# Optimization experiments

Hardware: AMD Instinct MI355X
Metric: run time of the kernel (lower is better)

## Reference

```python
import jax, jax.numpy as jnp
import numpy as np

LN_EPS = 1e-5
RMS_EPS = 1e-5

B, T, D = 4, 2048, 1024
H, DK, DV = 4, 256, 512            # head_k_dim = D/H, head_v_dim = expand_v * head_k_dim (expand_v=2)
KDIM, VDIM = H * DK, H * DV        # 1024, 2048
FFN = 4096                          # int(d_model * ffn_ratio)
CONV = 4


def _layernorm(x, w, b):
    mu = jnp.mean(x, -1, keepdims=True)
    var = jnp.mean(jnp.square(x - mu), -1, keepdims=True)
    return (x - mu) * jax.lax.rsqrt(var + LN_EPS) * w + b


def _short_conv_silu(x, w):
    # causal depthwise conv, kernel size K, then SiLU. x: [B,T,C], w: [C,K]
    K = w.shape[1]
    xp = jnp.pad(x, ((0, 0), (K - 1, 0), (0, 0)))
    y = sum(xp[:, i:i + x.shape[1], :] * w[:, i] for i in range(K))
    return jax.nn.silu(y)


def _l2norm(x):
    return x * jax.lax.rsqrt(jnp.sum(jnp.square(x), -1, keepdims=True) + 1e-6)


def _gated_delta_rule(q, k, v, g, beta):
    # q,k: [B,T,H,DK]; v: [B,T,H,DV]; g,beta: [B,T,H]
    # S_t = exp(g_t)*S_{t-1} + k_t (beta_t*(v_t - k_t^T exp(g_t) S_{t-1}))^T ; o_t = q_t^T S_t
    def step(S, inp):
        qt, kt, vt, gt, bt = inp
        S = S * jnp.exp(gt)[..., None, None]          # [B,H,DK,DV]
        mem = jnp.einsum('bhk,bhkv->bhv', kt, S)
        delta = (vt - mem) * bt[..., None]
        S = S + jnp.einsum('bhk,bhv->bhkv', kt, delta)
        o = jnp.einsum('bhk,bhkv->bhv', qt, S)
        return S, o
    S0 = jnp.zeros((q.shape[0], H, DK, DV), q.dtype)
    xs = (q.transpose(1, 0, 2, 3), k.transpose(1, 0, 2, 3), v.transpose(1, 0, 2, 3),
          g.transpose(1, 0, 2), beta.transpose(1, 0, 2))
    _, o = jax.lax.scan(step, S0, xs)
    return o.transpose(1, 0, 2, 3)  # [B,T,H,DV]


def setup_inputs() -> dict:
    key = jax.random.key(0)
    ks = jax.random.split(key, 24)
    n = lambda k, shp, s=0.02: jax.random.normal(k, shp, dtype=jnp.float32) * s
    return {
        'x': jax.random.normal(ks[0], (B, T, D), dtype=jnp.float32),
        'Wq': n(ks[1], (D, KDIM)), 'Wk': n(ks[2], (D, KDIM)), 'Wv': n(ks[3], (D, VDIM)),
        'Wa': n(ks[4], (D, H)), 'Wb': n(ks[5], (D, H)), 'Wg': n(ks[6], (D, VDIM)),
        'conv_q_w': n(ks[7], (KDIM, CONV), 0.2), 'conv_k_w': n(ks[8], (KDIM, CONV), 0.2),
        'conv_v_w': n(ks[9], (VDIM, CONV), 0.2),
        'A_log': jnp.log(jax.random.uniform(ks[10], (H,), minval=1.0, maxval=16.0, dtype=jnp.float32)),
        'dt_bias': jax.random.uniform(ks[11], (H,), minval=0.0, maxval=0.5, dtype=jnp.float32),
        'o_norm_w': jnp.ones((DV,), jnp.float32),
        'Wo': n(ks[12], (VDIM, D)),
        'ln1_w': jnp.ones((D,), jnp.float32), 'ln1_b': jnp.zeros((D,), jnp.float32),
        'ln2_w': jnp.ones((D,), jnp.float32), 'ln2_b': jnp.zeros((D,), jnp.float32),
        'ffn_w1': n(ks[13], (D, FFN)), 'ffn_b1': jnp.zeros((FFN,), jnp.float32),
        'ffn_w2': n(ks[14], (FFN, D)), 'ffn_b2': jnp.zeros((D,), jnp.float32),
    }


def reference(x, Wq, Wk, Wv, Wa, Wb, Wg, conv_q_w, conv_k_w, conv_v_w, A_log, dt_bias,
              o_norm_w, Wo, ln1_w, ln1_b, ln2_w, ln2_b, ffn_w1, ffn_b1, ffn_w2, ffn_b2):
    normed = _layernorm(x, ln1_w, ln1_b)
    q = _short_conv_silu(normed @ Wq, conv_q_w).reshape(B, T, H, DK)
    k = _short_conv_silu(normed @ Wk, conv_k_w).reshape(B, T, H, DK)
    v = _short_conv_silu(normed @ Wv, conv_v_w).reshape(B, T, H, DV)
    q = _l2norm(q) * (DK ** -0.5)
    k = _l2norm(k)
    g = -jnp.exp(A_log) * jax.nn.softplus(normed @ Wa + dt_bias)   # [B,T,H], negative
    beta = jax.nn.sigmoid(normed @ Wb)                              # [B,T,H]
    o = _gated_delta_rule(q, k, v, g, beta)                         # [B,T,H,DV]
    gate = (normed @ Wg).reshape(B, T, H, DV)
    o = o * jax.lax.rsqrt(jnp.mean(jnp.square(o), -1, keepdims=True) + RMS_EPS)
    o = o * o_norm_w * jax.nn.silu(gate)                            # gated RMSNorm
    x = x + o.reshape(B, T, VDIM) @ Wo
    h = _layernorm(x, ln2_w, ln2_b)
    ffn = jax.nn.gelu(h @ ffn_w1 + ffn_b1, approximate=False) @ ffn_w2 + ffn_b2
    return x + ffn
```

## Files before the change

### kernel.cpp

```cpp
#include <hip/hip_runtime.h>
#include <math.h>

#define B_    4
#define T_    2048
#define D_    1024
#define H_    4
#define DK_   256
#define DV_   512
#define KDIM_ 1024
#define VDIM_ 2048
#define FFN_  4096
#define BT_   8192

typedef unsigned short bf16;
typedef __attribute__((ext_vector_type(8))) short short8;
typedef __attribute__((ext_vector_type(4))) short short4v;
typedef __attribute__((ext_vector_type(4))) float f32x4;


__device__ __forceinline__ float sigmoidf_(float x) { return 1.f / (1.f + expf(-x)); }
__device__ __forceinline__ float siluf_(float x)    { return x / (1.f + expf(-x)); }
__device__ __forceinline__ float geluf_(float x)    { return 0.5f * x * (1.f + erff(x * 0.70710678118654752f)); }

__device__ __forceinline__ float bf2f(bf16 u) {
  union { unsigned int i; float f; } c; c.i = (unsigned int)u << 16; return c.f;
}
__device__ __forceinline__ bf16 f2bf(float f) {
  union { unsigned int i; float f; } c; c.f = f;
  unsigned int r = c.i + 0x7fffu + ((c.i >> 16) & 1u);
  return (bf16)(r >> 16);
}

__device__ __forceinline__ void gload16(const bf16* g, bf16* l) {
  __builtin_amdgcn_global_load_lds((__attribute__((address_space(1))) const void*)g,
                                   (__attribute__((address_space(3))) void*)l, 16, 0, 0);
}

__device__ __forceinline__ void storeC(float* p, float v) { *p = v; }
__device__ __forceinline__ void storeC(bf16* p, float v)  { *p = f2bf(v); }

__device__ __forceinline__ short8 ld76(const bf16* p) {
  union { short8 v; short4v h[2]; } u;
  u.h[0] = *(const short4v*)p;
  u.h[1] = *(const short4v*)(p + 4);
  return u.v;
}
__device__ __forceinline__ void st4bf(bf16* p, f32x4 v) {
  short4v o;
  o[0] = (short)f2bf(v[0]); o[1] = (short)f2bf(v[1]);
  o[2] = (short)f2bf(v[2]); o[3] = (short)f2bf(v[3]);
  *(short4v*)p = o;
}

__device__ __forceinline__ float block_sum256(float v, float* red) {
#pragma unroll
  for (int off = 32; off; off >>= 1) v += __shfl_xor(v, off, 64);
  __syncthreads();
  if ((threadIdx.x & 63) == 0) red[threadIdx.x >> 6] = v;
  __syncthreads();
  return red[0] + red[1] + red[2] + red[3];
}


__global__ __launch_bounds__(256) void sentinel_kernel(float* out, int n) {
  int i = blockIdx.x * 256 + threadIdx.x;
  if (i < n) out[i] = 12345.0f;
}


__global__ __launch_bounds__(256) void ln_kernel(const float* __restrict__ x,
                                                 const float* __restrict__ w,
                                                 const float* __restrict__ b,
                                                 bf16* __restrict__ y) {
  __shared__ float red[4];
  int row = blockIdx.x;
  const float* xr = x + (size_t)row * D_;
  float xv[4];
  float s = 0.f;
#pragma unroll
  for (int i = 0; i < 4; i++) { xv[i] = xr[threadIdx.x + 256 * i]; s += xv[i]; }
  float mean = block_sum256(s, red) * (1.f / D_);
  float s2 = 0.f;
#pragma unroll
  for (int i = 0; i < 4; i++) { float d = xv[i] - mean; s2 += d * d; }
  float var = block_sum256(s2, red) * (1.f / D_);
  float inv = rsqrtf(var + 1e-5f);
  bf16* yr = y + (size_t)row * D_;
#pragma unroll
  for (int i = 0; i < 4; i++) {
    int c = threadIdx.x + 256 * i;
    yr[c] = f2bf((xv[i] - mean) * inv * w[c] + b[c]);
  }
}


__global__ __launch_bounds__(256) void convT_kernel(const float* __restrict__ src,
                                                    bf16* __restrict__ dst,
                                                    int K, int N) {
  __shared__ float t[32][33];
  int n0 = blockIdx.x * 32, k0 = blockIdx.y * 32;
  int tx = threadIdx.x & 31, ty = threadIdx.x >> 5;
#pragma unroll
  for (int i = 0; i < 4; i++)
    t[ty + i * 8][tx] = src[(size_t)(k0 + ty + i * 8) * N + n0 + tx];
  __syncthreads();
#pragma unroll
  for (int i = 0; i < 4; i++)
    dst[(size_t)(n0 + ty + i * 8) * K + k0 + tx] = f2bf(t[tx][ty + i * 8]);
}


__global__ __launch_bounds__(256) void kT_kernel(const bf16* __restrict__ k16,
                                                 bf16* __restrict__ kT) {
  __shared__ bf16 tile[32][34];
  int t0 = blockIdx.x * 32;
  int d0 = blockIdx.y * 32;
  int bh = blockIdx.z;
  int b = bh >> 2, h = bh & 3;
  int tx = threadIdx.x & 31, ty = threadIdx.x >> 5;
#pragma unroll
  for (int i = 0; i < 4; i++)
    tile[ty + 8 * i][tx] = k16[(size_t)(b * T_ + t0 + ty + 8 * i) * KDIM_ + h * DK_ + d0 + tx];
  __syncthreads();
  int t = t0 + tx;
  int c = t >> 6, tb = (t >> 3) & 7, te = t & 7;
  size_t base = ((size_t)(bh * 32 + c) * 8 + tb) * 2048 + te;
#pragma unroll
  for (int i = 0; i < 4; i++)
    kT[base + (size_t)(d0 + ty + 8 * i) * 8] = tile[tx][ty + 8 * i];
}


template <typename TC>
__global__ __launch_bounds__(256) void gemm_mfma(const bf16* __restrict__ A,
                                                 const bf16* __restrict__ Bt,
                                                 const float* __restrict__ bias,
                                                 const float* __restrict__ res,
                                                 TC* __restrict__ C,
                                                 int N, int K, int flags) {
  __shared__ __align__(16) bf16 As[128 * 32];
  __shared__ __align__(16) bf16 Bs[128 * 32];
  int tid = threadIdx.x;
  int wave = tid >> 6, lane = tid & 63;
  int bm = blockIdx.y * 128, bn = blockIdx.x * 128;
  int wm = (wave >> 1) * 64, wn = (wave & 1) * 64;
  int lm = lane & 15;
  int quad = lane >> 4;

  f32x4 acc[4][4];
#pragma unroll
  for (int i = 0; i < 4; i++)
#pragma unroll
    for (int j = 0; j < 4; j++) acc[i][j] = (f32x4){0.f, 0.f, 0.f, 0.f};

  int srow = wave * 32 + (lane >> 2);
  int scol = (lane & 3) * 8;
  const bf16* ag = A  + (size_t)(bm + srow) * K + scol;
  const bf16* bg = Bt + (size_t)(bn + srow) * K + scol;
  bf16* al = As + wave * 32 * 32;
  bf16* bl = Bs + wave * 32 * 32;
  const size_t gstep = (size_t)16 * K;

  for (int k0 = 0; k0 < K; k0 += 32) {
    gload16(ag + k0,         al);
    gload16(ag + k0 + gstep, al + 16 * 32);
    gload16(bg + k0,         bl);
    gload16(bg + k0 + gstep, bl + 16 * 32);
    __syncthreads();

    short8 af[4], bf[4];
#pragma unroll
    for (int i = 0; i < 4; i++)
      af[i] = *(const short8*)&As[(wm + i * 16 + lm) * 32 + quad * 8];
#pragma unroll
    for (int j = 0; j < 4; j++)
      bf[j] = *(const short8*)&Bs[(wn + j * 16 + lm) * 32 + quad * 8];
#pragma unroll
    for (int i = 0; i < 4; i++)
#pragma unroll
      for (int j = 0; j < 4; j++)
        acc[i][j] = __builtin_amdgcn_mfma_f32_16x16x32_bf16(af[i], bf[j], acc[i][j], 0, 0, 0);
    __syncthreads();
  }

#pragma unroll
  for (int i = 0; i < 4; i++) {
    int row0 = bm + wm + i * 16 + quad * 4;
#pragma unroll
    for (int j = 0; j < 4; j++) {
      int col = bn + wn + j * 16 + lm;
      float badd = (flags & 1) ? bias[col] : 0.f;
#pragma unroll
      for (int r = 0; r < 4; r++) {
        float v = acc[i][j][r] + badd;
        if (flags & 2) v = geluf_(v);
        if (flags & 4) v += res[(size_t)(row0 + r) * N + col];
        storeC(&C[(size_t)(row0 + r) * N + col], v);
      }
    }
  }
}


__global__ __launch_bounds__(256) void ab_kernel(const bf16* __restrict__ normed,
                                                 const float* __restrict__ Wa,
                                                 const float* __restrict__ Wb,
                                                 const float* __restrict__ A_log,
                                                 const float* __restrict__ dt_bias,
                                                 float* __restrict__ g,
                                                 float* __restrict__ beta) {
  __shared__ float red[4];
  int row = blockIdx.x;
  const bf16* xr = normed + (size_t)row * D_;
  float aacc[4] = {}, bacc[4] = {};
#pragma unroll
  for (int i = 0; i < 4; i++) {
    int d = threadIdx.x + 256 * i;
    float xv = bf2f(xr[d]);
    float4 wa = *(const float4*)&Wa[d * 4];
    float4 wb = *(const float4*)&Wb[d * 4];
    aacc[0] += xv * wa.x; aacc[1] += xv * wa.y; aacc[2] += xv * wa.z; aacc[3] += xv * wa.w;
    bacc[0] += xv * wb.x; bacc[1] += xv * wb.y; bacc[2] += xv * wb.z; bacc[3] += xv * wb.w;
  }
  float sa[4], sb[4];
#pragma unroll
  for (int h = 0; h < 4; h++) {
    sa[h] = block_sum256(aacc[h], red);
    sb[h] = block_sum256(bacc[h], red);
  }
  if (threadIdx.x < 4) {
    int h = threadIdx.x;
    float xa = sa[h] + dt_bias[h];
    float sp = (xa > 20.f) ? xa : log1pf(expf(xa));
    g[row * 4 + h] = -expf(A_log[h]) * sp;
    beta[row * 4 + h] = sigmoidf_(sb[h]);
  }
}


__global__ __launch_bounds__(256) void conv_qk_kernel(const float* __restrict__ pre,
                                                      const float* __restrict__ convw,
                                                      bf16* __restrict__ out,
                                                      float scale) {
  __shared__ float red[4];
  int blk = blockIdx.x;
  int h = blk & 3;
  int bt = blk >> 2;
  int t = bt & (T_ - 1);
  int c = h * DK_ + threadIdx.x;
  float y = 0.f;
#pragma unroll
  for (int i = 0; i < 4; i++) {
    int tt = t + i - 3;
    if (tt >= 0) y += pre[(size_t)(bt + i - 3) * KDIM_ + c] * convw[c * 4 + i];
  }
  y = siluf_(y);
  float ss = block_sum256(y * y, red);
  y *= rsqrtf(ss + 1e-6f) * scale;
  out[(size_t)bt * KDIM_ + c] = f2bf(y);
}

__global__ __launch_bounds__(256) void conv_v_kernel(const float* __restrict__ pre,
                                                     const float* __restrict__ convw,
                                                     bf16* __restrict__ out) {
  int idx = blockIdx.x * 256 + threadIdx.x;
  int c = idx & (VDIM_ - 1);
  int bt = idx >> 11;
  int t = bt & (T_ - 1);
  float y = 0.f;
#pragma unroll
  for (int i = 0; i < 4; i++) {
    int tt = t + i - 3;
    if (tt >= 0) y += pre[(size_t)(bt + i - 3) * VDIM_ + c] * convw[c * 4 + i];
  }
  out[idx] = f2bf(siluf_(y));
}


#define SP  76
#define UBP 72
#define MTP 68

__global__ __launch_bounds__(256, 2) void delta_p1(const bf16* __restrict__ q,
                                                   const bf16* __restrict__ k,
                                                   const bf16* __restrict__ v,
                                                   const float* __restrict__ g,
                                                   const float* __restrict__ beta,
                                                   bf16* __restrict__ Pg,
                                                   bf16* __restrict__ Wg,
                                                   bf16* __restrict__ Yg,
                                                   float* __restrict__ gsc) {
  __shared__ bf16 Abf[64 * SP];
  __shared__ bf16 DTg[64 * SP];
  __shared__ __align__(8) bf16 MT[64 * MTP];
  __shared__ __align__(8) bf16 Ubt[64 * UBP];
  __shared__ float UbJ[16 * 64];
  __shared__ float Gc[64], Lm[64], Bt[64];

  int blk = blockIdx.x;
  int c = blk & 31, bh = blk >> 5;
  int b = bh >> 2, h = bh & 3;
  int tid = threadIdx.x;
  int wave = tid >> 6, lane = tid & 63;
  int lm = lane & 15, quad = lane >> 4;
  int r0 = c * 64;

  const bf16* kb = k + (size_t)b * T_ * KDIM_ + h * DK_;
  const bf16* qb = q + (size_t)b * T_ * KDIM_ + h * DK_;
  const bf16* vb = v + (size_t)b * T_ * VDIM_ + h * DV_;
  const float* gbp = g    + (size_t)b * T_ * H_ + h;
  const float* bbp = beta + (size_t)b * T_ * H_ + h;
  size_t cb = (size_t)bh * 32 + c;
  bf16* PgC = Pg + cb * 4096;
  bf16* WgC = Wg + cb * 64 * 512;
  bf16* YgC = Yg + cb * 64 * 256;

  if (wave == 0) {
    float gv = gbp[(size_t)(r0 + lane) * H_];
    float bv = bbp[(size_t)(r0 + lane) * H_];
#pragma unroll
    for (int d = 1; d < 64; d <<= 1) {
      float nn = __shfl_up(gv, (unsigned)d, 64);
      if (lane >= d) gv += nn;
    }
    Gc[lane] = gv; Lm[lane] = expf(gv); Bt[lane] = bv;
    gsc[cb * 64 + lane] = gv;
  }
  {
    int* dz = (int*)DTg;
#pragma unroll
    for (int i = 0; i < 10; i++) {
      int idx = tid + 256 * i;
      if (idx < 64 * SP / 2) dz[idx] = 0;
    }
  }
  __syncthreads();

  {
    f32x4 akk[4], aqk[4];
#pragma unroll
    for (int j = 0; j < 4; j++) { akk[j] = (f32x4){0.f,0.f,0.f,0.f}; aqk[j] = (f32x4){0.f,0.f,0.f,0.f}; }
    const bf16* krow = kb + (size_t)(r0 + 16 * wave + lm) * KDIM_;
    const bf16* qrow = qb + (size_t)(r0 + 16 * wave + lm) * KDIM_;
#pragma unroll
    for (int ks = 0; ks < 8; ks++) {
      short8 ak = *(const short8*)(krow + 8 * quad + 32 * ks);
      short8 aq = *(const short8*)(qrow + 8 * quad + 32 * ks);
#pragma unroll
      for (int j = 0; j < 4; j++) {
        short8 bk = *(const short8*)(kb + (size_t)(r0 + 16 * j + lm) * KDIM_ + 8 * quad + 32 * ks);
        akk[j] = __builtin_amdgcn_mfma_f32_16x16x32_bf16(ak, bk, akk[j], 0, 0, 0);
        aqk[j] = __builtin_amdgcn_mfma_f32_16x16x32_bf16(aq, bk, aqk[j], 0, 0, 0);
      }
    }
    float gi[4], bi[4];
#pragma unroll
    for (int r = 0; r < 4; r++) {
      int i = 16 * wave + 4 * quad + r;
      gi[r] = Gc[i]; bi[r] = Bt[i];
    }
#pragma unroll
    for (int j = 0; j < 4; j++) {
      int s = 16 * j + lm;
      float gs = Gc[s];
#pragma unroll
      for (int r = 0; r < 4; r++) {
        int i = 16 * wave + 4 * quad + r;
        float dec = expf(gi[r] - gs);
        Abf[(size_t)i * SP + s] = f2bf((s < i)  ? bi[r] * dec * akk[j][r] : 0.f);
        PgC[(size_t)i * 64 + s] = f2bf((s <= i) ? dec * aqk[j][r]        : 0.f);
      }
    }
  }
  __syncthreads();

#pragma unroll 1
  for (int j = 0; j < 4; j++) {
#pragma unroll
    for (int i = 0; i < 4; i++) {
      int idx = tid + 256 * i;
      int row = idx >> 6, col = idx & 63;
      UbJ[row * 64 + col] = (col == 16 * j + row) ? 1.f : 0.f;
    }
    __syncthreads();
    if (j > 0) {
      f32x4 racc = (f32x4){0.f, 0.f, 0.f, 0.f};
      int nk = (j == 3) ? 2 : 1;
      for (int ks = 0; ks < nk; ks++) {
        short8 aa = ld76(&Abf[(size_t)(16 * j + lm) * SP + 8 * quad + 32 * ks]);
        short8 bd = ld76(&DTg[(size_t)(16 * wave + lm) * SP + 8 * quad + 32 * ks]);
        racc = __builtin_amdgcn_mfma_f32_16x16x32_bf16(aa, bd, racc, 0, 0, 0);
      }
#pragma unroll
      for (int r = 0; r < 4; r++)
        UbJ[(4 * quad + r) * 64 + 16 * wave + lm] -= racc[r];
      __syncthreads();
    }
    if (wave == 0) {
      int tl = lane & 15, sg = lane >> 4;
      short4v ab4 = *(const short4v*)&Abf[(size_t)(16 * j + tl) * SP + 16 * j + 4 * sg];
      float av[4];
      av[0] = bf2f((bf16)ab4[0]); av[1] = bf2f((bf16)ab4[1]);
      av[2] = bf2f((bf16)ab4[2]); av[3] = bf2f((bf16)ab4[3]);
      float d[16];
#pragma unroll
      for (int t = 0; t < 16; t++) {
        float val = UbJ[t * 64 + lane];
#pragma unroll
        for (int s = 0; s < t; s++) {
          float ats = __shfl(av[s & 3], t + 16 * (s >> 2), 64);
          val -= ats * d[s];
        }
        d[t] = val;
        bf16 vb16 = f2bf(val);
        DTg[(size_t)lane * SP + 16 * j + t] = vb16;
        MT [(size_t)(16 * j + t) * MTP + lane] = vb16;
      }
    }
    __syncthreads();
  }

  int cg = 16 * wave + lm;
#pragma unroll 1
  for (int grp = 0; grp < 12; grp++) {
#pragma unroll
    for (int ti = 0; ti < 4; ti++) {
      short4v up;
#pragma unroll
      for (int r = 0; r < 4; r++) {
        int t = 16 * ti + 4 * quad + r;
        float val;
        if (grp < 8) val = Bt[t] * bf2f(vb[(size_t)(r0 + t) * VDIM_ + grp * 64 + cg]);
        else         val = Bt[t] * Lm[t] * bf2f(kb[(size_t)(r0 + t) * KDIM_ + (grp - 8) * 64 + cg]);
        up[r] = (short)f2bf(val);
      }
      *(short4v*)&Ubt[(size_t)cg * UBP + 16 * ti + 4 * quad] = up;
    }
    asm volatile("s_waitcnt lgkmcnt(0)" ::: "memory");
    __builtin_amdgcn_s_barrier();

    f32x4 racc[4];
#pragma unroll
    for (int jt = 0; jt < 4; jt++) racc[jt] = (f32x4){0.f, 0.f, 0.f, 0.f};
#pragma unroll
    for (int ks = 0; ks < 2; ks++) {
      short8 aM = ld76(&MT[(size_t)(16 * wave + lm) * MTP + 8 * quad + 32 * ks]);
#pragma unroll
      for (int jt = 0; jt < 4; jt++) {
        short8 bU = ld76(&Ubt[(size_t)(16 * jt + lm) * UBP + 8 * quad + 32 * ks]);
        racc[jt] = __builtin_amdgcn_mfma_f32_16x16x32_bf16(aM, bU, racc[jt], 0, 0, 0);
      }
    }
#pragma unroll
    for (int jt = 0; jt < 4; jt++) {
#pragma unroll
      for (int rr = 0; rr < 4; rr++) {
        int t = 16 * wave + 4 * quad + rr;
        int cc = 16 * jt + lm;
        if (grp < 8) WgC[(size_t)t * 512 + grp * 64 + cc]       = f2bf(racc[jt][rr]);
        else         YgC[(size_t)t * 256 + (grp - 8) * 64 + cc] = f2bf(racc[jt][rr]);
      }
    }
    asm volatile("s_waitcnt lgkmcnt(0)" ::: "memory");
    __builtin_amdgcn_s_barrier();
  }
}


#define SP2 264
#define SD  72

__global__ __launch_bounds__(256, 1) void delta_p2(const bf16* __restrict__ q,
                                                   const bf16* __restrict__ kT,
                                                   const bf16* __restrict__ Wg,
                                                   const bf16* __restrict__ Yg,
                                                   const bf16* __restrict__ Pg,
                                                   const float* __restrict__ gsc,
                                                   bf16* __restrict__ o) {
  __shared__ __align__(16) bf16 ST[32 * SP2];
  __shared__ __align__(16) bf16 dT[32 * SD];
  __shared__ __align__(16) bf16 dTe[32 * SD];
  __shared__ float Gc[64];
  __shared__ __align__(16) bf16 Ks[2][8 * 256 * 8];
  __shared__ __align__(16) bf16 Ws[2][64 * 32];

  int blk = blockIdx.x;
  int bh = blk & 15, vs = blk >> 4;
  int b = bh >> 2, h = bh & 3;
  int tid = threadIdx.x;
  int wave = tid >> 6, lane = tid & 63;
  int lm = lane & 15, quad = lane >> 4;
  int rt = wave;
  int v0 = vs * 32;

  const bf16* qb  = q  + (size_t)b * T_ * KDIM_ + h * DK_;
  const bf16* kTb = kT + (size_t)bh * 32 * 16384;
  const bf16* WgB = Wg + (size_t)bh * 32 * 32768 + (size_t)(tid >> 2) * 512 + v0 + (tid & 3) * 8;
  const bf16* PgB = Pg + (size_t)bh * 32 * 4096 + (size_t)(16 * rt + lm) * 64 + 8 * quad;
  bf16*       ob  = o  + (size_t)b * T_ * VDIM_ + h * DV_ + v0;

  f32x4 Sacc[4][2];
#pragma unroll
  for (int dd = 0; dd < 4; dd++)
#pragma unroll
    for (int cc = 0; cc < 2; cc++) Sacc[dd][cc] = (f32x4){0.f, 0.f, 0.f, 0.f};

#pragma unroll
  for (int i = 0; i < 8; i++)
    gload16(kTb + i * 2048 + tid * 8, Ks[0] + i * 2048 + wave * 512);
  gload16(WgB, Ws[0] + tid * 8);
  __builtin_amdgcn_sched_barrier(0);
  short8 pfn[2];
  pfn[0] = *(const short8*)(PgB);
  pfn[1] = *(const short8*)(PgB + 32);
  __builtin_amdgcn_sched_barrier(0);
  float gnext = gsc[(size_t)bh * 2048 + lane], gnn = 0.f;
  short8 qfr[8], yfr[8];
  {
    const bf16* qrow = qb + (size_t)(16 * rt + lm) * KDIM_;
    const bf16* yrow = Yg + (size_t)bh * 32 * 16384 + (size_t)(16 * rt + lm) * 256;
#pragma unroll
    for (int kf = 0; kf < 8; kf++) {
      qfr[kf] = *(const short8*)(qrow + 8 * quad + 32 * kf);
      yfr[kf] = *(const short8*)(yrow + 8 * quad + 32 * kf);
    }
  }

  for (int c = 0; c < 32; c++) {
    const int r0 = c * 64;
    const int idx = c & 1;
    const bf16* Ksb = Ks[idx];
    const bf16* Wsb = Ws[idx];
    bf16* Ksn = Ks[idx ^ 1];
    bf16* Wsn = Ws[idx ^ 1];

#pragma unroll
    for (int dd = 0; dd < 4; dd++)
#pragma unroll
      for (int cc = 0; cc < 2; cc++)
        st4bf(&ST[(size_t)(16 * cc + lm) * SP2 + 16 * (4 * wave + dd) + 4 * quad], Sacc[dd][cc]);
    Gc[lane] = gnext;
    asm volatile("s_waitcnt lgkmcnt(0)" ::: "memory");
    __builtin_amdgcn_s_barrier();

    f32x4 Yacc[2], Oacc[2];
#pragma unroll
    for (int cc = 0; cc < 2; cc++) { Yacc[cc] = (f32x4){0.f,0.f,0.f,0.f}; Oacc[cc] = (f32x4){0.f,0.f,0.f,0.f}; }
#pragma unroll
    for (int cc = 0; cc < 2; cc++) {
      short8 Bs[8];
#pragma unroll
      for (int kf = 0; kf < 8; kf++)
        Bs[kf] = *(const short8*)&ST[(size_t)(16 * cc + lm) * SP2 + 8 * quad + 32 * kf];
#pragma unroll
      for (int kf = 0; kf < 8; kf++) {
        Yacc[cc] = __builtin_amdgcn_mfma_f32_16x16x32_bf16(yfr[kf], Bs[kf], Yacc[cc], 0, 0, 0);
        Oacc[cc] = __builtin_amdgcn_mfma_f32_16x16x32_bf16(qfr[kf], Bs[kf], Oacc[cc], 0, 0, 0);
      }
    }
    __builtin_amdgcn_sched_barrier(0);

    {
      int cn = (c + 1) & 31;
      size_t cbn = (size_t)bh * 32 + cn;
      const bf16* slab = kTb + (size_t)cn * 16384;
#pragma unroll
      for (int i = 0; i < 8; i++)
        gload16(slab + i * 2048 + tid * 8, Ksn + i * 2048 + wave * 512);
      gload16(WgB + (size_t)cn * 32768, Wsn + tid * 8);
      __builtin_amdgcn_sched_barrier(0);
      gnn = gsc[cbn * 64 + lane];
      const bf16* qrow = qb + (size_t)(cn * 64 + 16 * rt + lm) * KDIM_;
      const bf16* yrow = Yg + cbn * 16384 + (size_t)(16 * rt + lm) * 256;
#pragma unroll
      for (int kf = 0; kf < 8; kf++) {
        qfr[kf] = *(const short8*)(qrow + 8 * quad + 32 * kf);
        yfr[kf] = *(const short8*)(yrow + 8 * quad + 32 * kf);
      }
    }
    __builtin_amdgcn_sched_barrier(0);

    asm volatile("" : : "v"(*(const int*)&pfn[0]), "v"(*(const int*)&pfn[1]) : "memory");
    __builtin_amdgcn_sched_barrier(0);
    float g63 = Gc[63];
    float lamv[4], erv[4];
#pragma unroll
    for (int rr = 0; rr < 4; rr++) {
      float gr = Gc[16 * rt + 4 * quad + rr];
      lamv[rr] = __expf(gr);
      erv[rr]  = __expf(g63 - gr);
    }
#pragma unroll
    for (int cc = 0; cc < 2; cc++) {
      short4v dpack, depack;
#pragma unroll
      for (int rr = 0; rr < 4; rr++) {
        int row = 16 * rt + 4 * quad + rr;
        float dv = bf2f(Wsb[row * 32 + 16 * cc + lm]) - Yacc[cc][rr];
        Oacc[cc][rr] *= lamv[rr];
        dpack[rr]  = (short)f2bf(dv);
        depack[rr] = (short)f2bf(dv * erv[rr]);
      }
      *(short4v*)&dT [(size_t)(16 * cc + lm) * SD + 16 * rt + 4 * quad] = dpack;
      *(short4v*)&dTe[(size_t)(16 * cc + lm) * SD + 16 * rt + 4 * quad] = depack;
    }
    asm volatile("s_waitcnt lgkmcnt(0)" ::: "memory");
    __builtin_amdgcn_s_barrier();

    float lend = __expf(g63);
    short8 Be[2][2];
#pragma unroll
    for (int cc = 0; cc < 2; cc++)
#pragma unroll
      for (int kf = 0; kf < 2; kf++)
        Be[cc][kf] = ld76(&dTe[(size_t)(16 * cc + lm) * SD + 8 * quad + 32 * kf]);
#pragma unroll
    for (int dd = 0; dd < 4; dd++) {
      int Dt = 4 * wave + dd;
#pragma unroll
      for (int cc = 0; cc < 2; cc++) {
        f32x4 s = Sacc[dd][cc];
        s[0] *= lend; s[1] *= lend; s[2] *= lend; s[3] *= lend;
#pragma unroll
        for (int kf = 0; kf < 2; kf++) {
          short8 ka = *(const short8*)&Ksb[((size_t)(quad + 4 * kf) * 256 + 16 * Dt + lm) * 8];
          s = __builtin_amdgcn_mfma_f32_16x16x32_bf16(ka, Be[cc][kf], s, 0, 0, 0);
        }
        Sacc[dd][cc] = s;
      }
    }

#pragma unroll
    for (int cc = 0; cc < 2; cc++) {
#pragma unroll
      for (int kf = 0; kf < 2; kf++) {
        short8 bd = ld76(&dT[(size_t)(16 * cc + lm) * SD + 8 * quad + 32 * kf]);
        Oacc[cc] = __builtin_amdgcn_mfma_f32_16x16x32_bf16(pfn[kf], bd, Oacc[cc], 0, 0, 0);
      }
#pragma unroll
      for (int rr = 0; rr < 4; rr++) {
        int row = 16 * rt + 4 * quad + rr;
        ob[(size_t)(r0 + row) * VDIM_ + 16 * cc + lm] = f2bf(Oacc[cc][rr]);
      }
    }
    __builtin_amdgcn_sched_barrier(0);

    {
      int cn = (c + 1) & 31;
      const bf16* pc = PgB + (size_t)cn * 4096;
      pfn[0] = *(const short8*)(pc);
      pfn[1] = *(const short8*)(pc + 32);
    }
    gnext = gnn;
    asm volatile("s_waitcnt lgkmcnt(0)" ::: "memory");
    __builtin_amdgcn_s_barrier();
  }
}


__global__ __launch_bounds__(256) void gated_rms_kernel(bf16* __restrict__ o,
                                                        const bf16* __restrict__ gate,
                                                        const float* __restrict__ onw) {
  __shared__ float red[4];
  int blk = blockIdx.x;
  int h = blk & 3;
  int bt = blk >> 2;
  size_t base = (size_t)bt * VDIM_ + h * DV_;
  int tid = threadIdx.x;
  float o1 = bf2f(o[base + tid]), o2 = bf2f(o[base + tid + 256]);
  float ss = block_sum256(o1 * o1 + o2 * o2, red);
  float s = rsqrtf(ss * (1.f / DV_) + 1e-5f);
  float g1 = bf2f(gate[base + tid]), g2 = bf2f(gate[base + tid + 256]);
  o[base + tid]       = f2bf(o1 * s * onw[tid] * siluf_(g1));
  o[base + tid + 256] = f2bf(o2 * s * onw[tid + 256] * siluf_(g2));
}


extern "C" void kernel_launch(void* const* d_in, const int* in_sizes, int n_in,
                              void* d_out, int out_size, void* d_ws, size_t ws_size,
                              hipStream_t stream) {
  const float* x        = (const float*)d_in[0];
  const float* Wq       = (const float*)d_in[1];
  const float* Wk       = (const float*)d_in[2];
  const float* Wv       = (const float*)d_in[3];
  const float* Wa       = (const float*)d_in[4];
  const float* Wb       = (const float*)d_in[5];
  const float* Wg       = (const float*)d_in[6];
  const float* conv_q_w = (const float*)d_in[7];
  const float* conv_k_w = (const float*)d_in[8];
  const float* conv_v_w = (const float*)d_in[9];
  const float* A_log    = (const float*)d_in[10];
  const float* dt_bias  = (const float*)d_in[11];
  const float* o_norm_w = (const float*)d_in[12];
  const float* Wo       = (const float*)d_in[13];
  const float* ln1_w    = (const float*)d_in[14];
  const float* ln1_b    = (const float*)d_in[15];
  const float* ln2_w    = (const float*)d_in[16];
  const float* ln2_b    = (const float*)d_in[17];
  const float* ffn_w1   = (const float*)d_in[18];
  const float* ffn_b1   = (const float*)d_in[19];
  const float* ffn_w2   = (const float*)d_in[20];
  const float* ffn_b2   = (const float*)d_in[21];

  size_t required = (size_t)218 << 20;
  if (ws_size < required) {
    sentinel_kernel<<<(out_size + 255) / 256, 256, 0, stream>>>((float*)d_out, out_size);
    return;
  }

  char* base = (char*)d_ws;
  float* pre    = (float*)(base);
  bf16*  normed = (bf16*)(base + ((size_t)64  << 20));
  bf16*  q16    = (bf16*)(base + ((size_t)80  << 20));
  bf16*  k16    = (bf16*)(base + ((size_t)96  << 20));
  bf16*  v16    = (bf16*)(base + ((size_t)112 << 20));
  bf16*  g16    = (bf16*)(base + ((size_t)144 << 20));
  bf16*  o16    = (bf16*)(base + ((size_t)176 << 20));
  bf16*  wslot  = (bf16*)(base + ((size_t)208 << 20));
  float* gvec   = (float*)(base + ((size_t)216 << 20));
  float* bvec   = gvec + (size_t)BT_ * H_;
  float* gsc    = (float*)(base + ((size_t)217 << 20));
  bf16*  Yg     = (bf16*)(base);
  bf16*  Wgb    = (bf16*)(base + ((size_t)16 << 20));
  bf16*  Pg     = (bf16*)(base + ((size_t)48 << 20));
  bf16*  kTg    = (bf16*)(base + ((size_t)52 << 20));
  float* x2     = (float*)(base);
  bf16*  hb16   = (bf16*)(base + ((size_t)64  << 20));
  bf16*  ffn1   = (bf16*)(base + ((size_t)80  << 20));

  ln_kernel<<<BT_, 256, 0, stream>>>(x, ln1_w, ln1_b, normed);

  convT_kernel<<<dim3(KDIM_ / 32, D_ / 32), 256, 0, stream>>>(Wq, wslot, D_, KDIM_);
  gemm_mfma<float><<<dim3(KDIM_ / 128, BT_ / 128), 256, 0, stream>>>(normed, wslot, nullptr, nullptr, pre, KDIM_, D_, 0);
  conv_qk_kernel<<<BT_ * H_, 256, 0, stream>>>(pre, conv_q_w, q16, 0.0625f);

  convT_kernel<<<dim3(KDIM_ / 32, D_ / 32), 256, 0, stream>>>(Wk, wslot, D_, KDIM_);
  gemm_mfma<float><<<dim3(KDIM_ / 128, BT_ / 128), 256, 0, stream>>>(normed, wslot, nullptr, nullptr, pre, KDIM_, D_, 0);
  conv_qk_kernel<<<BT_ * H_, 256, 0, stream>>>(pre, conv_k_w, k16, 1.0f);

  convT_kernel<<<dim3(VDIM_ / 32, D_ / 32), 256, 0, stream>>>(Wv, wslot, D_, VDIM_);
  gemm_mfma<float><<<dim3(VDIM_ / 128, BT_ / 128), 256, 0, stream>>>(normed, wslot, nullptr, nullptr, pre, VDIM_, D_, 0);
  conv_v_kernel<<<(BT_ * VDIM_) / 256, 256, 0, stream>>>(pre, conv_v_w, v16);

  convT_kernel<<<dim3(VDIM_ / 32, D_ / 32), 256, 0, stream>>>(Wg, wslot, D_, VDIM_);
  gemm_mfma<bf16><<<dim3(VDIM_ / 128, BT_ / 128), 256, 0, stream>>>(normed, wslot, nullptr, nullptr, g16, VDIM_, D_, 0);

  ab_kernel<<<BT_, 256, 0, stream>>>(normed, Wa, Wb, A_log, dt_bias, gvec, bvec);

  kT_kernel<<<dim3(T_ / 32, DK_ / 32, 16), 256, 0, stream>>>(k16, kTg);
  delta_p1<<<512, 256, 0, stream>>>(q16, k16, v16, gvec, bvec, Pg, Wgb, Yg, gsc);
  delta_p2<<<256, 256, 0, stream>>>(q16, kTg, Wgb, Yg, Pg, gsc, o16);

  gated_rms_kernel<<<BT_ * H_, 256, 0, stream>>>(o16, g16, o_norm_w);

  convT_kernel<<<dim3(D_ / 32, VDIM_ / 32), 256, 0, stream>>>(Wo, wslot, VDIM_, D_);
  gemm_mfma<float><<<dim3(D_ / 128, BT_ / 128), 256, 0, stream>>>(o16, wslot, nullptr, x, x2, D_, VDIM_, 4);

  ln_kernel<<<BT_, 256, 0, stream>>>(x2, ln2_w, ln2_b, hb16);

  convT_kernel<<<dim3(FFN_ / 32, D_ / 32), 256, 0, stream>>>(ffn_w1, wslot, D_, FFN_);
  gemm_mfma<bf16><<<dim3(FFN_ / 128, BT_ / 128), 256, 0, stream>>>(hb16, wslot, ffn_b1, nullptr, ffn1, FFN_, D_, 1 | 2);
  convT_kernel<<<dim3(D_ / 32, FFN_ / 32), 256, 0, stream>>>(ffn_w2, wslot, FFN_, D_);
  gemm_mfma<float><<<dim3(D_ / 128, BT_ / 128), 256, 0, stream>>>(ffn1, wslot, ffn_b2, x2, (float*)d_out, D_, FFN_, 1 | 4);
}
```

Baseline: 1.101 ms.

## Double-buffer GEMM LDS tiles and remap blocks for XCD locality

The generic MFMA GEMM now keeps two LDS buffers per operand and issues the global-to-LDS loads for the next K slice before computing on the current one. This leaves one barrier per iteration instead of two and overlaps load latency with MFMA work. Block ids are also remapped so that consecutive ids, which are spread across the 8 XCDs, map to row tiles in a way meant to improve L2 reuse per XCD. The cost is double the LDS per block, which may lower occupancy, and the remap assumes the grid's y dimension is a multiple of 8.

```diff
diff --git a/kernel.cpp b/kernel.cpp
--- a/kernel.cpp
+++ b/kernel.cpp
@@ -138,11 +138,19 @@
                                                  const float* __restrict__ res,
                                                  TC* __restrict__ C,
                                                  int N, int K, int flags) {
-  __shared__ __align__(16) bf16 As[128 * 32];
-  __shared__ __align__(16) bf16 Bs[128 * 32];
+  __shared__ __align__(16) bf16 As[2][128 * 32];
+  __shared__ __align__(16) bf16 Bs[2][128 * 32];
   int tid = threadIdx.x;
   int wave = tid >> 6, lane = tid & 63;
-  int bm = blockIdx.y * 128, bn = blockIdx.x * 128;
+
+  int nbx = gridDim.x;
+  int id  = blockIdx.y * nbx + blockIdx.x;
+  int xcd = id & 7;
+  int g   = id >> 3;
+  int bx  = g % nbx;
+  int by  = xcd + 8 * (g / nbx);
+  int bm = by * 128, bn = bx * 128;
+
   int wm = (wave >> 1) * 64, wn = (wave & 1) * 64;
   int lm = lane & 15;
   int quad = lane >> 4;
@@ -157,30 +165,41 @@
   int scol = (lane & 3) * 8;
   const bf16* ag = A  + (size_t)(bm + srow) * K + scol;
   const bf16* bg = Bt + (size_t)(bn + srow) * K + scol;
-  bf16* al = As + wave * 32 * 32;
-  bf16* bl = Bs + wave * 32 * 32;
   const size_t gstep = (size_t)16 * K;
-
+  int woff = wave * 1024;
+
+  gload16(ag,         &As[0][woff]);
+  gload16(ag + gstep, &As[0][woff + 512]);
+  gload16(bg,         &Bs[0][woff]);
+  gload16(bg + gstep, &Bs[0][woff + 512]);
+  __syncthreads();
+
+  int cur = 0;
   for (int k0 = 0; k0 < K; k0 += 32) {
-    gload16(ag + k0,         al);
-    gload16(ag + k0 + gstep, al + 16 * 32);
-    gload16(bg + k0,         bl);
-    gload16(bg + k0 + gstep, bl + 16 * 32);
-    __syncthreads();
+    if (k0 + 32 < K) {
+      int nb = cur ^ 1;
+      gload16(ag + k0 + 32,         &As[nb][woff]);
+      gload16(ag + k0 + 32 + gstep, &As[nb][woff + 512]);
+      gload16(bg + k0 + 32,         &Bs[nb][woff]);
+      gload16(bg + k0 + 32 + gstep, &Bs[nb][woff + 512]);
+    }
+    __builtin_amdgcn_sched_barrier(0);
 
     short8 af[4], bf[4];
 #pragma unroll
     for (int i = 0; i < 4; i++)
-      af[i] = *(const short8*)&As[(wm + i * 16 + lm) * 32 + quad * 8];
+      af[i] = *(const short8*)&As[cur][(wm + i * 16 + lm) * 32 + quad * 8];
 #pragma unroll
     for (int j = 0; j < 4; j++)
-      bf[j] = *(const short8*)&Bs[(wn + j * 16 + lm) * 32 + quad * 8];
+      bf[j] = *(const short8*)&Bs[cur][(wn + j * 16 + lm) * 32 + quad * 8];
 #pragma unroll
     for (int i = 0; i < 4; i++)
 #pragma unroll
       for (int j = 0; j < 4; j++)
         acc[i][j] = __builtin_amdgcn_mfma_f32_16x16x32_bf16(af[i], bf[j], acc[i][j], 0, 0, 0);
+
     __syncthreads();
+    cur ^= 1;
   }
 
 #pragma unroll
@@ -548,14 +567,14 @@
     for (int cc = 0; cc < 2; cc++) { Yacc[cc] = (f32x4){0.f,0.f,0.f,0.f}; Oacc[cc] = (f32x4){0.f,0.f,0.f,0.f}; }
 #pragma unroll
     for (int cc = 0; cc < 2; cc++) {
-      short8 Bs[8];
+      short8 Bs2[8];
 #pragma unroll
       for (int kf = 0; kf < 8; kf++)
-        Bs[kf] = *(const short8*)&ST[(size_t)(16 * cc + lm) * SP2 + 8 * quad + 32 * kf];
+        Bs2[kf] = *(const short8*)&ST[(size_t)(16 * cc + lm) * SP2 + 8 * quad + 32 * kf];
 #pragma unroll
       for (int kf = 0; kf < 8; kf++) {
-        Yacc[cc] = __builtin_amdgcn_mfma_f32_16x16x32_bf16(yfr[kf], Bs[kf], Yacc[cc], 0, 0, 0);
-        Oacc[cc] = __builtin_amdgcn_mfma_f32_16x16x32_bf16(qfr[kf], Bs[kf], Oacc[cc], 0, 0, 0);
+        Yacc[cc] = __builtin_amdgcn_mfma_f32_16x16x32_bf16(yfr[kf], Bs2[kf], Yacc[cc], 0, 0, 0);
+        Oacc[cc] = __builtin_amdgcn_mfma_f32_16x16x32_bf16(qfr[kf], Bs2[kf], Oacc[cc], 0, 0, 0);
       }
     }
     __builtin_amdgcn_sched_barrier(0);
```

New measurement: 1.050 ms. -4.6%, faster.
